# Kernel tuning notes

Measured on AMD Instinct MI355X. Metric: run time of the kernel, lower is better.

Reference implementation:

```python
import jax, jax.numpy as jnp
import numpy as np

H_IN = 1024
H_OUT = 1024
P = 512
DT_MIN = 0.004
DT_MAX = 0.1
STEP_RESCALE = 1.0
MIN_NEG = 1e-3
EPS_LAM = 1e-6
EPS_DIV = 1e-9
CLIP_MAX = 20.0


def _hippo_lambda_raw(p):
    # Mirrors TorchS5.__init__ HiPPO-LegS-style symmetric init.
    idx = np.arange(p, dtype=np.float64)
    Pv = np.sqrt(1.0 + 2.0 * idx)
    A = np.tril(Pv[:, None] * Pv[None, :]) - np.diag(idx)
    A = -A
    Pr = np.sqrt(idx + 0.5)
    S = A + Pr[:, None] * Pr[None, :]
    S_sym = 0.5 * (S + S.T)
    eig = np.linalg.eigvalsh(S_sym).astype(np.float32)
    lambda_init = -np.clip(np.abs(eig), 1e-3, None)
    raw = -np.log(np.expm1(np.clip(-lambda_init, 1e-6, None)))
    return jnp.asarray(raw, dtype=jnp.float32)


def setup_inputs() -> dict:
    key = jax.random.key(0)
    ku, kt, kb, kc = jax.random.split(key, 4)
    Bsz, L = 16, 1024
    u = jax.random.normal(ku, (Bsz, L, H_IN), dtype=jnp.float32)
    timesteps = jax.random.uniform(kt, (Bsz, L), dtype=jnp.float32)
    Lambda_raw = _hippo_lambda_raw(P)
    log_step_init = 0.5 * (np.log(DT_MIN) + np.log(DT_MAX))
    log_step = jnp.full((P,), log_step_init, dtype=jnp.float32)
    # kaiming_uniform_(a=sqrt(5)) -> U(-1/sqrt(fan_in), 1/sqrt(fan_in))
    Bmat = jax.random.uniform(kb, (P, H_IN), dtype=jnp.float32,
                              minval=-1.0, maxval=1.0) / np.sqrt(H_IN)
    Cmat = jax.random.uniform(kc, (H_OUT, P), dtype=jnp.float32,
                              minval=-1.0, maxval=1.0) / np.sqrt(P)
    Dvec = jnp.zeros((H_IN,), dtype=jnp.float32)  # H_in == H_out path
    return {"u": u, "timesteps": timesteps, "Lambda_raw": Lambda_raw,
            "log_step": log_step, "B": Bmat, "C": Cmat, "D": Dvec}


def reference(u, timesteps, Lambda_raw, log_step, B, C, D):
    # u: [B,L,H_in], timesteps: [B,L]
    Bu = jnp.einsum('ph,blh->blp', B, u)                      # [B,L,P]
    step_vec = STEP_RESCALE * jnp.exp(log_step)               # [P]
    Lam = -(jax.nn.softplus(Lambda_raw) + MIN_NEG)            # [P]
    Delta = jnp.maximum(step_vec[None, None, :] * timesteps[..., None], 0.0)
    A_bar = jnp.exp(jnp.minimum(Lam[None, None, :] * Delta, CLIP_MAX))
    # zoh gamma: (exp(Lam*Delta)-1)/Lam, fallback Delta near Lam=0
    gamma = jnp.where(jnp.abs(Lam)[None, None, :] > EPS_LAM,
                      (A_bar - 1.0) / Lam[None, None, :], Delta)
    b_seq = gamma * Bu
    A_cum = jnp.cumprod(A_bar, axis=1)                        # [B,L,P]
    z = b_seq / (A_cum + EPS_DIV)
    s = jnp.cumsum(z, axis=1)
    x_seq = A_cum * s
    ys = jnp.einsum('hp,blp->blh', C, x_seq) + D * u          # [B,L,H_out]
    return ys
```

## Files before the change

kernel.cpp:

```cpp
#include <hip/hip_runtime.h>
#include <cstdint>
#include <cstddef>

#define H_IN   1024
#define H_OUTD 1024
#define PDIM   512
#define BSZ    16
#define LSEQ   1024
#define BLM    (BSZ * LSEQ)
#define CCH    32
#define CLEN   32

typedef __bf16 bf16_t;
typedef __bf16 bf16x8 __attribute__((ext_vector_type(8)));
typedef float  floatx4 __attribute__((ext_vector_type(4)));

__device__ __forceinline__ unsigned short f2bf(float f) {
    unsigned u = __float_as_uint(f);
    u = u + 0x7fffu + ((u >> 16) & 1u);
    return (unsigned short)(u >> 16);
}
__device__ __forceinline__ float bf2f(unsigned short s) {
    return __uint_as_float((unsigned)s << 16);
}

__device__ __forceinline__ void gl_lds16(const void* g, void* l) {
    __builtin_amdgcn_global_load_lds(
        (const __attribute__((address_space(1))) void*)g,
        (__attribute__((address_space(3))) void*)l, 16, 0, 0);
}

#define NU4 (BLM * H_IN / 4)
#define NB4 (PDIM * H_IN / 4)
#define NC4 (H_OUTD * PDIM / 4)
__global__ void setup_kernel(const float* __restrict__ Lraw,
                             const float* __restrict__ lstep,
                             float* __restrict__ stepv,
                             float* __restrict__ lamv,
                             const float4* __restrict__ Usrc,
                             ushort4* __restrict__ Udst,
                             const float4* __restrict__ Bsrc,
                             ushort4* __restrict__ Bdst,
                             const float4* __restrict__ Csrc,
                             ushort4* __restrict__ Cdst) {
    const int gid = blockIdx.x * 256 + threadIdx.x;
    if (gid < PDIM) {
        stepv[gid] = expf(lstep[gid]);
        float x = Lraw[gid];
        float sp = fmaxf(x, 0.0f) + log1pf(expf(-fabsf(x)));
        lamv[gid] = -(sp + 1e-3f);
    }
    if (gid < NU4) {
        float4 v = Usrc[gid];
        ushort4 o;
        o.x = f2bf(v.x); o.y = f2bf(v.y); o.z = f2bf(v.z); o.w = f2bf(v.w);
        Udst[gid] = o;
    } else {
        const int g2 = gid - NU4;
        if (g2 < NB4) {
            float4 v = Bsrc[g2];
            ushort4 o;
            o.x = f2bf(v.x); o.y = f2bf(v.y); o.z = f2bf(v.z); o.w = f2bf(v.w);
            Bdst[g2] = o;
        } else if (g2 < NB4 + NC4) {
            const int g3 = g2 - NB4;
            float4 v = Csrc[g3];
            ushort4 o;
            o.x = f2bf(v.x); o.y = f2bf(v.y); o.z = f2bf(v.z); o.w = f2bf(v.w);
            Cdst[g3] = o;
        }
    }
}

template<int EPI, int OUTBF, int GXL>
__global__ __launch_bounds__(256, 4)
void gemm_nt(const bf16_t* __restrict__ A, const bf16_t* __restrict__ Bm,
             float* __restrict__ Cf, unsigned short* __restrict__ Cb,
             int M, int N, int K,
             const float* __restrict__ Dv, const unsigned short* __restrict__ U) {
    __shared__ bf16_t As[128 * 32];
    __shared__ bf16_t Bs[128 * 32];

    const int i     = blockIdx.x;
    const int n_blk = (i >> 3) & ((1 << GXL) - 1);
    const int m_blk = ((i >> (3 + GXL)) << 3) | (i & 7);
    const int m0    = m_blk << 7;
    const int n0    = n_blk << 7;

    const int tid  = threadIdx.x;
    const int lane = tid & 63;
    const int w    = tid >> 6;
    const int wm   = (w & 1) << 6;
    const int wn   = (w >> 1) << 6;
    const int r16  = lane & 15;
    const int q    = lane >> 4;
    const int fsw  = (q ^ (r16 & 3)) << 3;

    const int srow = lane >> 2;
    const int seg  = (lane & 3) ^ (srow & 3);
    const int c0   = w * 32;
    const int c1   = c0 + 16;

    const bf16_t* gA0 = A  + (size_t)(m0 + c0 + srow) * K + seg * 8;
    const bf16_t* gA1 = A  + (size_t)(m0 + c1 + srow) * K + seg * 8;
    const bf16_t* gB0 = Bm + (size_t)(n0 + c0 + srow) * K + seg * 8;
    const bf16_t* gB1 = Bm + (size_t)(n0 + c1 + srow) * K + seg * 8;
    bf16_t* lA0 = &As[c0 * 32];
    bf16_t* lA1 = &As[c1 * 32];
    bf16_t* lB0 = &Bs[c0 * 32];
    bf16_t* lB1 = &Bs[c1 * 32];

    floatx4 acc[4][4] = {};

    for (int k0 = 0; k0 < K; k0 += 32) {
        gl_lds16(gA0 + k0, lA0);
        gl_lds16(gA1 + k0, lA1);
        gl_lds16(gB0 + k0, lB0);
        gl_lds16(gB1 + k0, lB1);
        __syncthreads();

        bf16x8 af[4], bfr[4];
#pragma unroll
        for (int ii = 0; ii < 4; ++ii) {
            af[ii]  = *(const bf16x8*)&As[(wm + ii * 16 + r16) * 32 + fsw];
            bfr[ii] = *(const bf16x8*)&Bs[(wn + ii * 16 + r16) * 32 + fsw];
        }
#pragma unroll
        for (int mi = 0; mi < 4; ++mi)
#pragma unroll
            for (int ni = 0; ni < 4; ++ni)
                acc[mi][ni] = __builtin_amdgcn_mfma_f32_16x16x32_bf16(
                    af[mi], bfr[ni], acc[mi][ni], 0, 0, 0);
        __syncthreads();
    }

    float dn[4];
    if (EPI == 1) {
#pragma unroll
        for (int ni = 0; ni < 4; ++ni) dn[ni] = Dv[n0 + wn + ni * 16 + r16];
    }
#pragma unroll
    for (int mi = 0; mi < 4; ++mi) {
#pragma unroll
        for (int e = 0; e < 4; ++e) {
            const int m = m0 + wm + mi * 16 + q * 4 + e;
#pragma unroll
            for (int ni = 0; ni < 4; ++ni) {
                const int n = n0 + wn + ni * 16 + r16;
                const size_t idx = (size_t)m * N + n;
                float v = acc[mi][ni][e];
                if (EPI == 1) v += dn[ni] * bf2f(U[idx]);
                if (OUTBF == 1) Cb[idx] = f2bf(v);
                else            Cf[idx] = v;
            }
        }
    }
}

__global__ __launch_bounds__(512)
void scan_part1(const unsigned short* __restrict__ Bu, const float* __restrict__ ts,
                const float* __restrict__ stepv, const float* __restrict__ lamv,
                float* __restrict__ Pagg, float* __restrict__ Sagg) {
    const int c = blockIdx.x;
    const int b = blockIdx.y;
    const int p = threadIdx.x;

    const float lam  = lamv[p];
    const float stp  = stepv[p];
    const float rlam = 1.0f / lam;
    const bool  lam_big = fabsf(lam) > 1e-6f;

    const unsigned short* bu = Bu + ((size_t)b * LSEQ + c * CLEN) * PDIM + p;
    const float* tb = ts + b * LSEQ + c * CLEN;

    float P = 1.0f, S = 0.0f;
#pragma unroll 8
    for (int i = 0; i < CLEN; ++i) {
        float t     = tb[i];
        float delta = fmaxf(stp * t, 0.0f);
        float e     = fminf(lam * delta, 20.0f);
        float abar  = __expf(e);
        float gamma = lam_big ? (abar - 1.0f) * rlam : delta;
        S = fmaf(abar, S, gamma * bf2f(bu[(size_t)i * PDIM]));
        P *= abar;
    }
    const size_t o = ((size_t)b * CCH + c) * PDIM + p;
    Pagg[o] = P;
    Sagg[o] = S;
}

__global__ __launch_bounds__(512)
void scan_part23(const unsigned short* __restrict__ Bu, const float* __restrict__ ts,
                 const float* __restrict__ stepv, const float* __restrict__ lamv,
                 const float* __restrict__ Pagg, const float* __restrict__ Sagg,
                 unsigned short* __restrict__ Xbf) {
    const int c = blockIdx.x;
    const int b = blockIdx.y;
    const int p = threadIdx.x;

    const float lam  = lamv[p];
    const float stp  = stepv[p];
    const float rlam = 1.0f / lam;
    const bool  lam_big = fabsf(lam) > 1e-6f;

    float x = 0.0f;
    for (int cc = 0; cc < c; ++cc) {
        const size_t o = ((size_t)b * CCH + cc) * PDIM + p;
        x = fmaf(Pagg[o], x, Sagg[o]);
    }

    const unsigned short* bu = Bu + ((size_t)b * LSEQ + c * CLEN) * PDIM + p;
    const float* tb = ts + b * LSEQ + c * CLEN;
    unsigned short* xo = Xbf + ((size_t)b * LSEQ + c * CLEN) * PDIM + p;

#pragma unroll 8
    for (int i = 0; i < CLEN; ++i) {
        float t     = tb[i];
        float delta = fmaxf(stp * t, 0.0f);
        float e     = fminf(lam * delta, 20.0f);
        float abar  = __expf(e);
        float gamma = lam_big ? (abar - 1.0f) * rlam : delta;
        x = fmaf(abar, x, gamma * bf2f(bu[(size_t)i * PDIM]));
        xo[(size_t)i * PDIM] = f2bf(x);
    }
}

extern "C" void kernel_launch(void* const* d_in, const int* in_sizes, int n_in,
                              void* d_out, int out_size, void* d_ws, size_t ws_size,
                              hipStream_t stream) {
    (void)in_sizes; (void)n_in; (void)out_size; (void)ws_size;
    const float* u  = (const float*)d_in[0];
    const float* ts = (const float*)d_in[1];
    const float* Lr = (const float*)d_in[2];
    const float* ls = (const float*)d_in[3];
    const float* Bm = (const float*)d_in[4];
    const float* Cm = (const float*)d_in[5];
    const float* Dv = (const float*)d_in[6];
    float* out = (float*)d_out;

    char* ws = (char*)d_ws;
    bf16_t*         u_bf = (bf16_t*)(ws);
    bf16_t*         B_bf = (bf16_t*)(ws + (32u << 20));
    bf16_t*         C_bf = (bf16_t*)(ws + (33u << 20));
    unsigned short* Bu   = (unsigned short*)(ws + (34u << 20));
    unsigned short* X_bf = (unsigned short*)(ws + (50u << 20));
    float*          Pagg = (float*)(ws + (66u << 20));
    float*          Sagg = (float*)(ws + (67u << 20));
    float*          stepv= (float*)(ws + (69u << 20));
    float*          lamv = stepv + PDIM;

    setup_kernel<<<(NU4 + NB4 + NC4) / 256, 256, 0, stream>>>(
        Lr, ls, stepv, lamv,
        (const float4*)u,  (ushort4*)u_bf,
        (const float4*)Bm, (ushort4*)B_bf,
        (const float4*)Cm, (ushort4*)C_bf);

    gemm_nt<0, 1, 2><<<512, 256, 0, stream>>>(
        u_bf, B_bf, nullptr, Bu, BLM, PDIM, H_IN, nullptr, nullptr);

    scan_part1<<<dim3(CCH, BSZ), 512, 0, stream>>>(Bu, ts, stepv, lamv, Pagg, Sagg);
    scan_part23<<<dim3(CCH, BSZ), 512, 0, stream>>>(Bu, ts, stepv, lamv,
                                                    Pagg, Sagg, X_bf);

    gemm_nt<1, 0, 3><<<1024, 256, 0, stream>>>(
        (const bf16_t*)X_bf, C_bf, out, nullptr, BLM, H_OUTD, PDIM, Dv,
        (const unsigned short*)u_bf);
}
```

Measured before the change: 195.8 us.

## Double-buffer GEMM LDS tiles and tree-combine chunk carries in scan

The GEMM kernel now keeps two LDS tile buffers and issues the global-to-LDS loads for the next K-slice before computing on the current one, dropping one barrier per iteration so loads overlap the MFMA work. The scan's chunk-carry prefix loop is unrolled by four, with the affine (P,S) pairs combined as a small tree, which shortens the dependent FMA chain and lets more loads be in flight. Doubling LDS per block (to 32KB) may lower occupancy at the 4-blocks launch bound. The reassociated carry arithmetic slightly changes float rounding.

Measured after the change: 192.8 us. About the same (-1.5%).

```diff
diff --git a/kernel.cpp b/kernel.cpp
--- a/kernel.cpp
+++ b/kernel.cpp
@@ -78,8 +78,8 @@
              float* __restrict__ Cf, unsigned short* __restrict__ Cb,
              int M, int N, int K,
              const float* __restrict__ Dv, const unsigned short* __restrict__ U) {
-    __shared__ bf16_t As[128 * 32];
-    __shared__ bf16_t Bs[128 * 32];
+    __shared__ bf16_t As[2 * 128 * 32];
+    __shared__ bf16_t Bs[2 * 128 * 32];
 
     const int i     = blockIdx.x;
     const int n_blk = (i >> 3) & ((1 << GXL) - 1);
@@ -112,18 +112,29 @@
 
     floatx4 acc[4][4] = {};
 
+    gl_lds16(gA0, lA0);
+    gl_lds16(gA1, lA1);
+    gl_lds16(gB0, lB0);
+    gl_lds16(gB1, lB1);
+    __syncthreads();
+
+    int cur = 0;
     for (int k0 = 0; k0 < K; k0 += 32) {
-        gl_lds16(gA0 + k0, lA0);
-        gl_lds16(gA1 + k0, lA1);
-        gl_lds16(gB0 + k0, lB0);
-        gl_lds16(gB1 + k0, lB1);
-        __syncthreads();
-
+        const int nxt = cur ^ 1;
+        if (k0 + 32 < K) {
+            gl_lds16(gA0 + k0 + 32, lA0 + nxt * 4096);
+            gl_lds16(gA1 + k0 + 32, lA1 + nxt * 4096);
+            gl_lds16(gB0 + k0 + 32, lB0 + nxt * 4096);
+            gl_lds16(gB1 + k0 + 32, lB1 + nxt * 4096);
+        }
+
+        const bf16_t* rA = As + cur * 4096;
+        const bf16_t* rB = Bs + cur * 4096;
         bf16x8 af[4], bfr[4];
 #pragma unroll
         for (int ii = 0; ii < 4; ++ii) {
-            af[ii]  = *(const bf16x8*)&As[(wm + ii * 16 + r16) * 32 + fsw];
-            bfr[ii] = *(const bf16x8*)&Bs[(wn + ii * 16 + r16) * 32 + fsw];
+            af[ii]  = *(const bf16x8*)&rA[(wm + ii * 16 + r16) * 32 + fsw];
+            bfr[ii] = *(const bf16x8*)&rB[(wn + ii * 16 + r16) * 32 + fsw];
         }
 #pragma unroll
         for (int mi = 0; mi < 4; ++mi)
@@ -131,7 +142,9 @@
             for (int ni = 0; ni < 4; ++ni)
                 acc[mi][ni] = __builtin_amdgcn_mfma_f32_16x16x32_bf16(
                     af[mi], bfr[ni], acc[mi][ni], 0, 0, 0);
+
         __syncthreads();
+        cur = nxt;
     }
 
     float dn[4];
@@ -203,10 +216,22 @@
     const float rlam = 1.0f / lam;
     const bool  lam_big = fabsf(lam) > 1e-6f;
 
+    const float* Pb = Pagg + (size_t)b * CCH * PDIM + p;
+    const float* Sb = Sagg + (size_t)b * CCH * PDIM + p;
     float x = 0.0f;
-    for (int cc = 0; cc < c; ++cc) {
-        const size_t o = ((size_t)b * CCH + cc) * PDIM + p;
-        x = fmaf(Pagg[o], x, Sagg[o]);
+    int cc = 0;
+    for (; cc + 4 <= c; cc += 4) {
+        float p0 = Pb[(size_t)(cc + 0) * PDIM], s0 = Sb[(size_t)(cc + 0) * PDIM];
+        float p1 = Pb[(size_t)(cc + 1) * PDIM], s1 = Sb[(size_t)(cc + 1) * PDIM];
+        float p2 = Pb[(size_t)(cc + 2) * PDIM], s2 = Sb[(size_t)(cc + 2) * PDIM];
+        float p3 = Pb[(size_t)(cc + 3) * PDIM], s3 = Sb[(size_t)(cc + 3) * PDIM];
+        float p01 = p0 * p1, s01 = fmaf(s0, p1, s1);
+        float p23 = p2 * p3, s23 = fmaf(s2, p3, s3);
+        float pq  = p01 * p23, sq = fmaf(s01, p23, s23);
+        x = fmaf(pq, x, sq);
+    }
+    for (; cc < c; ++cc) {
+        x = fmaf(Pb[(size_t)cc * PDIM], x, Sb[(size_t)cc * PDIM]);
     }
 
     const unsigned short* bu = Bu + ((size_t)b * LSEQ + c * CLEN) * PDIM + p;
```
